# Kernel optimization log

Measured on AMD Instinct MI355X. Metric: run time of the kernel, lower is better.

## Reference

```python
import jax, jax.numpy as jnp
import numpy as np


def setup_inputs() -> dict:
    key = jax.random.key(0)
    ks = jax.random.split(key, 7)
    C = 256
    Cqk = C // 8  # 32
    B, D, H, W = 4, 16, 16, 16
    s_in = 1.0 / np.sqrt(C)  # conv1x1 fan_in = C
    return {
        "x": jax.random.normal(ks[0], (B, C, D, H, W), dtype=jnp.float32),
        "Wq": jax.random.uniform(ks[1], (Cqk, C), jnp.float32, -s_in, s_in),
        "bq": jax.random.uniform(ks[2], (Cqk,), jnp.float32, -s_in, s_in),
        "Wk": jax.random.uniform(ks[3], (Cqk, C), jnp.float32, -s_in, s_in),
        "bk": jax.random.uniform(ks[4], (Cqk,), jnp.float32, -s_in, s_in),
        "Wv": jax.random.uniform(ks[5], (C, C), jnp.float32, -s_in, s_in),
        "bv": jax.random.uniform(ks[6], (C,), jnp.float32, -s_in, s_in),
    }


def reference(x, Wq, bq, Wk, bk, Wv, bv):
    B, C, D, H, W = x.shape
    N = D * H * W
    xf = x.reshape(B, C, N)  # [B, C, N]
    # 1x1x1 convs == per-voxel GEMMs over the channel dim
    q = jnp.einsum('oc,bcn->bon', Wq, xf) + bq[None, :, None]  # [B, Cqk, N]
    k = jnp.einsum('oc,bcn->bon', Wk, xf) + bk[None, :, None]  # [B, Cqk, N]
    v = jnp.einsum('oc,bcn->bon', Wv, xf) + bv[None, :, None]  # [B, C, N]
    # attention[b, n, m] = softmax_m( q[:, n] . k[:, m] )
    scores = jnp.einsum('bcn,bcm->bnm', q, k)  # [B, N, N]
    attn = jax.nn.softmax(scores, axis=-1)
    # out = value @ attention^T  -> out[b, c, n] = sum_m v[b,c,m] * attn[b,n,m]
    out = jnp.einsum('bcm,bnm->bcn', v, attn)
    return x + out.reshape(B, C, D, H, W)
```

## Files before the change

### kernel.cpp

```cpp
#include <hip/hip_runtime.h>
#include <math.h>

#define B_   4
#define C_   256
#define CQK  32
#define N_   4096
#define TQ   64
#define TM   128
#define HIT2 (N_ / TM)
#define PSS  136
#define XTS  264

typedef __attribute__((ext_vector_type(8))) short short8;
typedef __attribute__((ext_vector_type(4))) short short4v;
typedef __attribute__((ext_vector_type(4))) float f32x4;
typedef __attribute__((ext_vector_type(2))) unsigned int uint2v;

#if __has_builtin(__builtin_amdgcn_exp2f)
#define EXP2F(x) __builtin_amdgcn_exp2f(x)
#else
#define EXP2F(x) exp2f(x)
#endif

__device__ __forceinline__ unsigned short f2bf(float f) {
    unsigned u = __builtin_bit_cast(unsigned, f);
    u += 0x7fffu + ((u >> 16) & 1u);
    return (unsigned short)(u >> 16);
}
__device__ __forceinline__ float bf2f(unsigned short s) {
    return __builtin_bit_cast(float, (unsigned)s << 16);
}
__device__ __forceinline__ unsigned pack2bf(float a, float b) {
    unsigned ua = __builtin_bit_cast(unsigned, a) + 0x8000u;
    unsigned ub = __builtin_bit_cast(unsigned, b) + 0x8000u;
#if __has_builtin(__builtin_amdgcn_perm)
    return __builtin_amdgcn_perm(ub, ua, 0x07060302u);
#else
    return (ua >> 16) | (ub & 0xffff0000u);
#endif
}

__global__ __launch_bounds__(256) void cvt_w(
    const float* __restrict__ Wq, const float* __restrict__ bq,
    const float* __restrict__ Wk, const float* __restrict__ bk,
    const float* __restrict__ Wv, const float* __restrict__ bv,
    unsigned short* __restrict__ wbf, float* __restrict__ biasf)
{
    const float LOG2E = 1.4426950408889634f;
    const int r = blockIdx.x;
    const int t = threadIdx.x;
    const float* src = (r < 32) ? (Wq + r * C_)
                     : (r < 64) ? (Wk + (r - 32) * C_)
                                : (Wv + (r - 64) * C_);
    const float scale = (r < 32) ? LOG2E : 1.0f;
    wbf[r * C_ + t] = f2bf(src[t] * scale);
    if (t == 0)
        biasf[r] = (r < 32) ? bq[r] * LOG2E : (r < 64) ? bk[r - 32] : bv[r - 64];
}

__global__ __launch_bounds__(256, 2) void proj_qkv(
    const float* __restrict__ x, const unsigned short* __restrict__ wbf,
    const float* __restrict__ biasf,
    unsigned short* __restrict__ qb, unsigned short* __restrict__ kb,
    unsigned short* __restrict__ vb)
{
    __shared__ __align__(16) unsigned short xT[64 * XTS];
    __shared__ __align__(16) unsigned short qks[64 * 72];

    const int t    = threadIdx.x;
    const int w    = t >> 6;
    const int lane = t & 63;
    const int quad = lane >> 4;
    const int c16  = lane & 15;
    const int n0   = blockIdx.x * 64;
    const int b    = blockIdx.y;

#pragma unroll
    for (int p = 0; p < 16; ++p) {
        const int c  = (t >> 2) + 64 * (p >> 2);
        const int nq = (t & 3) + 4 * (p & 3);
        const f32x4 xv = *(const f32x4*)&x[((size_t)(b * C_) + c) * N_ + n0 + 4 * nq];
#pragma unroll
        for (int j = 0; j < 4; ++j)
            xT[(4 * nq + j) * XTS + c] = f2bf(xv[j]);
    }
    __syncthreads();

    f32x4 acc[5][4];
#pragma unroll
    for (int i = 0; i < 5; ++i)
#pragma unroll
        for (int nt = 0; nt < 4; ++nt) acc[i][nt] = (f32x4){0.f, 0.f, 0.f, 0.f};

    const unsigned short* wr = wbf + (size_t)(80 * w + c16) * C_ + quad * 8;

#pragma unroll
    for (int ks = 0; ks < 8; ++ks) {
        short8 af[5], bf[4];
#pragma unroll
        for (int i = 0; i < 5; ++i)
            af[i] = *(const short8*)(wr + (size_t)(16 * i) * C_ + 32 * ks);
#pragma unroll
        for (int nt = 0; nt < 4; ++nt)
            bf[nt] = *(const short8*)&xT[(16 * nt + c16) * XTS + ks * 32 + quad * 8];
#pragma unroll
        for (int i = 0; i < 5; ++i)
#pragma unroll
            for (int nt = 0; nt < 4; ++nt)
                acc[i][nt] = __builtin_amdgcn_mfma_f32_16x16x32_bf16(af[i], bf[nt], acc[i][nt], 0, 0, 0);
    }

#pragma unroll
    for (int i = 0; i < 5; ++i) {
        const int OT = 5 * w + i;
        const int obase = OT * 16 + 4 * quad;
        const f32x4 bv4 = *(const f32x4*)&biasf[obase];
#pragma unroll
        for (int nt = 0; nt < 4; ++nt) {
            const int n = n0 + 16 * nt + c16;
            float vals[4];
#pragma unroll
            for (int r = 0; r < 4; ++r) vals[r] = acc[i][nt][r] + bv4[r];
            if (OT >= 4) {
#pragma unroll
                for (int r = 0; r < 4; ++r)
                    vb[((size_t)(b * C_) + obase + r - 64) * N_ + n] = f2bf(vals[r]);
            } else {
                const int row = 16 * nt + c16;
                const int col = (OT < 2 ? 0 : 32) + (OT & 1) * 16 + 4 * quad;
                short4v pk;
#pragma unroll
                for (int r = 0; r < 4; ++r) pk[r] = (short)f2bf(vals[r]);
                *(short4v*)&qks[row * 72 + col] = pk;
            }
        }
    }
    __syncthreads();
    if (w < 2) {
        unsigned short* dst = w ? kb : qb;
        const int coff = w ? 32 : 0;
#pragma unroll
        for (int h = 0; h < 4; ++h) {
            const int n = 16 * h + (lane >> 2);
            const int c = (lane & 3) * 8;
            const short8 v = *(const short8*)&qks[n * 72 + coff + c];
            *(short8*)(dst + ((size_t)(b * N_) + n0 + n) * 32 + c) = v;
        }
    }
}

__global__ __launch_bounds__(512, 2) void attn_kernel(
    const unsigned short* __restrict__ qg,
    const unsigned short* __restrict__ kg,
    const unsigned short* __restrict__ vg,
    const float* __restrict__ x,
    float* __restrict__ out)
{
    __shared__ __align__(16) unsigned short ks[TM * 40];
    __shared__ __align__(16) unsigned short vs[C_ * TM];
    __shared__ __align__(16) unsigned short ps[TQ * PSS];
    __shared__ float ls[8 * TQ];
    __shared__ float linv[TQ];

    const int t    = threadIdx.x;
    const int w    = t >> 6;
    const int lane = t & 63;
    const int quad = lane >> 4;
    const int c16  = lane & 15;
    const int flat = blockIdx.x;
    const int b    = flat & 3;
    const int q0   = (flat >> 2) * TQ;
    const int cs = w & 3;
    const int pg = w >> 2;

    const unsigned short* kbase = kg + (size_t)(b * N_) * 32;
    const unsigned short* vbase = vg + (size_t)(b * C_) * N_;

    short8 bq[4];
#pragma unroll
    for (int g = 0; g < 4; ++g)
        bq[g] = *(const short8*)(qg + ((size_t)(b * N_) + q0 + 16 * g + c16) * 32 + quad * 8);

    const int vcr = t >> 4, vj = t & 15;
    const int kn = t >> 2, kseg = t & 3;

    short8 vpre[8], kpre;
#pragma unroll
    for (int p = 0; p < 8; ++p)
        vpre[p] = *(const short8*)(vbase + (size_t)(vcr + 32 * p) * N_ + vj * 8);
    kpre = *(const short8*)(kbase + (size_t)kn * 32 + kseg * 8);

    f32x4 O[4][2];
#pragma unroll
    for (int ct = 0; ct < 4; ++ct)
#pragma unroll
        for (int qt = 0; qt < 2; ++qt) O[ct][qt] = (f32x4){0.f, 0.f, 0.f, 0.f};

    float lacc[4] = {0.f, 0.f, 0.f, 0.f};

#pragma unroll 1
    for (int it = 0; it < HIT2; ++it) {
#pragma unroll
        for (int p = 0; p < 8; ++p) {
            const int c = vcr + 32 * p;
            *(short8*)&vs[c * TM + 8 * (vj ^ (c & 15))] = vpre[p];
        }
        *(short8*)&ks[kn * 40 + kseg * 8] = kpre;
        __syncthreads();

        const short8 ak = *(const short8*)&ks[(16 * w + c16) * 40 + quad * 8];
        const f32x4 z = {0.f, 0.f, 0.f, 0.f};
        f32x4 sf[4];
#pragma unroll
        for (int g = 0; g < 4; ++g)
            sf[g] = __builtin_amdgcn_mfma_f32_16x16x32_bf16(ak, bq[g], z, 0, 0, 0);

#pragma unroll
        for (int g = 0; g < 4; ++g) {
            float p[4];
#pragma unroll
            for (int r = 0; r < 4; ++r) p[r] = EXP2F(sf[g][r]);
            lacc[g] += (p[0] + p[1]) + (p[2] + p[3]);
            uint2v u;
            u.x = pack2bf(p[0], p[1]);
            u.y = pack2bf(p[2], p[3]);
            *(uint2v*)&ps[(16 * g + c16) * PSS + w * 16 + 4 * quad] = u;
        }
        __syncthreads();

        if (it < HIT2 - 1) {
            const int kv0n = (it + 1) * TM;
#pragma unroll
            for (int p = 0; p < 8; ++p)
                vpre[p] = *(const short8*)(vbase + (size_t)(vcr + 32 * p) * N_ + kv0n + vj * 8);
            kpre = *(const short8*)(kbase + (size_t)(kv0n + kn) * 32 + kseg * 8);
        }

        short8 bp[2][4];
#pragma unroll
        for (int qt = 0; qt < 2; ++qt)
#pragma unroll
            for (int s = 0; s < 4; ++s)
                bp[qt][s] = *(const short8*)&ps[(32 * pg + 16 * qt + c16) * PSS + 32 * s + 8 * quad];
#pragma unroll
        for (int s = 0; s < 4; ++s)
#pragma unroll
            for (int ct = 0; ct < 4; ++ct) {
                const int c = 64 * cs + 16 * ct + c16;
                const short8 av = *(const short8*)&vs[c * TM + 8 * ((4 * s + quad) ^ (c & 15))];
#pragma unroll
                for (int qt = 0; qt < 2; ++qt)
                    O[ct][qt] = __builtin_amdgcn_mfma_f32_16x16x32_bf16(av, bp[qt][s], O[ct][qt], 0, 0, 0);
            }
        __syncthreads();
    }

#pragma unroll
    for (int g = 0; g < 4; ++g) {
        lacc[g] += __shfl_xor(lacc[g], 16);
        lacc[g] += __shfl_xor(lacc[g], 32);
    }
    if (quad == 0) {
#pragma unroll
        for (int g = 0; g < 4; ++g)
            ls[w * TQ + 16 * g + c16] = lacc[g];
    }
    __syncthreads();
    if (w == 0) {
        float s = 0.f;
#pragma unroll
        for (int j = 0; j < 8; ++j) s += ls[j * TQ + lane];
        linv[lane] = 1.0f / s;
    }
    __syncthreads();

    const float* xb = x + (size_t)(b * C_) * N_;
    float* ob = out + (size_t)(b * C_) * N_;
    float li[2];
#pragma unroll
    for (int qt = 0; qt < 2; ++qt) li[qt] = linv[32 * pg + 16 * qt + c16];
#pragma unroll
    for (int ct = 0; ct < 4; ++ct)
#pragma unroll
        for (int qt = 0; qt < 2; ++qt) {
            const int n = q0 + 32 * pg + 16 * qt + c16;
#pragma unroll
            for (int r = 0; r < 4; ++r) {
                const int c = 64 * cs + 16 * ct + 4 * quad + r;
                const size_t idx = (size_t)c * N_ + n;
                ob[idx] = xb[idx] + O[ct][qt][r] * li[qt];
            }
        }
}

extern "C" void kernel_launch(void* const* d_in, const int* in_sizes, int n_in,
                              void* d_out, int out_size, void* d_ws, size_t ws_size,
                              hipStream_t stream) {
    const float* x  = (const float*)d_in[0];
    const float* Wq = (const float*)d_in[1];
    const float* bq = (const float*)d_in[2];
    const float* Wk = (const float*)d_in[3];
    const float* bk = (const float*)d_in[4];
    const float* Wv = (const float*)d_in[5];
    const float* bv = (const float*)d_in[6];
    float* out = (float*)d_out;

    unsigned short* ws16 = (unsigned short*)d_ws;
    unsigned short* qb  = ws16;
    unsigned short* kb  = qb + (size_t)B_ * N_ * 32;
    unsigned short* vb  = kb + (size_t)B_ * N_ * 32;
    unsigned short* wbf = vb + (size_t)B_ * C_ * N_;
    float* biasf = (float*)(wbf + 320 * C_);

    cvt_w<<<dim3(320), 256, 0, stream>>>(Wq, bq, Wk, bk, Wv, bv, wbf, biasf);
    proj_qkv<<<dim3(N_ / 64, B_), 256, 0, stream>>>(x, wbf, biasf, qb, kb, vb);
    attn_kernel<<<dim3(256), 512, 0, stream>>>(qb, kb, vb, x, out);
}
```

Baseline: 154.6 us.

## Halve query and key tiles in attention kernel to double grid occupancy

Reduces the attention query tile to 32 and key tile to 64, doubles the grid to 512 blocks and raises launch bounds to four blocks per CU. Warp roles are remapped so four warps compute the scores and each warp accumulates one 16-query strip across its channel slice. This aims to fill more CUs and raise occupancy to hide latency. In exchange, V is reloaded from global memory twice as often per query, and barriers are more frequent relative to the MFMA work.

```diff
diff --git a/kernel.cpp b/kernel.cpp
--- a/kernel.cpp
+++ b/kernel.cpp
@@ -5,10 +5,10 @@
 #define C_   256
 #define CQK  32
 #define N_   4096
-#define TQ   64
-#define TM   128
-#define HIT2 (N_ / TM)
-#define PSS  136
+#define TQ   32
+#define TM   64
+#define HIT3 (N_ / TM)
+#define PSS  72
 #define XTS  264
 
 typedef __attribute__((ext_vector_type(8))) short short8;
@@ -149,7 +149,7 @@
     }
 }
 
-__global__ __launch_bounds__(512, 2) void attn_kernel(
+__global__ __launch_bounds__(512, 4) void attn_kernel(
     const unsigned short* __restrict__ qg,
     const unsigned short* __restrict__ kg,
     const unsigned short* __restrict__ vg,
@@ -159,7 +159,7 @@
     __shared__ __align__(16) unsigned short ks[TM * 40];
     __shared__ __align__(16) unsigned short vs[C_ * TM];
     __shared__ __align__(16) unsigned short ps[TQ * PSS];
-    __shared__ float ls[8 * TQ];
+    __shared__ float ls[4 * TQ];
     __shared__ float linv[TQ];
 
     const int t    = threadIdx.x;
@@ -170,127 +170,105 @@
     const int flat = blockIdx.x;
     const int b    = flat & 3;
     const int q0   = (flat >> 2) * TQ;
+    const int f   = w & 3;
+    const int qg_ = w >> 2;
     const int cs = w & 3;
     const int pg = w >> 2;
 
     const unsigned short* kbase = kg + (size_t)(b * N_) * 32;
     const unsigned short* vbase = vg + (size_t)(b * C_) * N_;
 
-    short8 bq[4];
-#pragma unroll
-    for (int g = 0; g < 4; ++g)
-        bq[g] = *(const short8*)(qg + ((size_t)(b * N_) + q0 + 16 * g + c16) * 32 + quad * 8);
-
-    const int vcr = t >> 4, vj = t & 15;
+    const short8 bq = *(const short8*)(qg + ((size_t)(b * N_) + q0 + 16 * qg_ + c16) * 32 + quad * 8);
+
+    const int vc0 = t >> 3, vj = t & 7;
     const int kn = t >> 2, kseg = t & 3;
 
-    short8 vpre[8], kpre;
-#pragma unroll
-    for (int p = 0; p < 8; ++p)
-        vpre[p] = *(const short8*)(vbase + (size_t)(vcr + 32 * p) * N_ + vj * 8);
-    kpre = *(const short8*)(kbase + (size_t)kn * 32 + kseg * 8);
-
-    f32x4 O[4][2];
-#pragma unroll
-    for (int ct = 0; ct < 4; ++ct)
-#pragma unroll
-        for (int qt = 0; qt < 2; ++qt) O[ct][qt] = (f32x4){0.f, 0.f, 0.f, 0.f};
-
-    float lacc[4] = {0.f, 0.f, 0.f, 0.f};
+    short8 vpre[4], kpre;
+#pragma unroll
+    for (int p = 0; p < 4; ++p)
+        vpre[p] = *(const short8*)(vbase + (size_t)(vc0 + 64 * p) * N_ + vj * 8);
+    if (t < 256)
+        kpre = *(const short8*)(kbase + (size_t)kn * 32 + kseg * 8);
+
+    f32x4 O[4];
+#pragma unroll
+    for (int ct = 0; ct < 4; ++ct) O[ct] = (f32x4){0.f, 0.f, 0.f, 0.f};
+
+    float lacc = 0.f;
 
 #pragma unroll 1
-    for (int it = 0; it < HIT2; ++it) {
-#pragma unroll
-        for (int p = 0; p < 8; ++p) {
-            const int c = vcr + 32 * p;
-            *(short8*)&vs[c * TM + 8 * (vj ^ (c & 15))] = vpre[p];
-        }
-        *(short8*)&ks[kn * 40 + kseg * 8] = kpre;
+    for (int it = 0; it < HIT3; ++it) {
+#pragma unroll
+        for (int p = 0; p < 4; ++p) {
+            const int c = vc0 + 64 * p;
+            *(short8*)&vs[c * TM + 8 * (vj ^ (c & 7))] = vpre[p];
+        }
+        if (t < 256)
+            *(short8*)&ks[kn * 40 + kseg * 8] = kpre;
         __syncthreads();
 
-        const short8 ak = *(const short8*)&ks[(16 * w + c16) * 40 + quad * 8];
+        const short8 ak = *(const short8*)&ks[(16 * f + c16) * 40 + quad * 8];
         const f32x4 z = {0.f, 0.f, 0.f, 0.f};
-        f32x4 sf[4];
-#pragma unroll
-        for (int g = 0; g < 4; ++g)
-            sf[g] = __builtin_amdgcn_mfma_f32_16x16x32_bf16(ak, bq[g], z, 0, 0, 0);
-
-#pragma unroll
-        for (int g = 0; g < 4; ++g) {
+        const f32x4 sf = __builtin_amdgcn_mfma_f32_16x16x32_bf16(ak, bq, z, 0, 0, 0);
+
+        {
             float p[4];
 #pragma unroll
-            for (int r = 0; r < 4; ++r) p[r] = EXP2F(sf[g][r]);
-            lacc[g] += (p[0] + p[1]) + (p[2] + p[3]);
+            for (int r = 0; r < 4; ++r) p[r] = EXP2F(sf[r]);
+            lacc += (p[0] + p[1]) + (p[2] + p[3]);
             uint2v u;
             u.x = pack2bf(p[0], p[1]);
             u.y = pack2bf(p[2], p[3]);
-            *(uint2v*)&ps[(16 * g + c16) * PSS + w * 16 + 4 * quad] = u;
+            *(uint2v*)&ps[(16 * qg_ + c16) * PSS + f * 16 + 4 * quad] = u;
         }
         __syncthreads();
 
-        if (it < HIT2 - 1) {
+        if (it < HIT3 - 1) {
             const int kv0n = (it + 1) * TM;
 #pragma unroll
-            for (int p = 0; p < 8; ++p)
-                vpre[p] = *(const short8*)(vbase + (size_t)(vcr + 32 * p) * N_ + kv0n + vj * 8);
-            kpre = *(const short8*)(kbase + (size_t)(kv0n + kn) * 32 + kseg * 8);
-        }
-
-        short8 bp[2][4];
-#pragma unroll
-        for (int qt = 0; qt < 2; ++qt)
-#pragma unroll
-            for (int s = 0; s < 4; ++s)
-                bp[qt][s] = *(const short8*)&ps[(32 * pg + 16 * qt + c16) * PSS + 32 * s + 8 * quad];
-#pragma unroll
-        for (int s = 0; s < 4; ++s)
+            for (int p = 0; p < 4; ++p)
+                vpre[p] = *(const short8*)(vbase + (size_t)(vc0 + 64 * p) * N_ + kv0n + vj * 8);
+            if (t < 256)
+                kpre = *(const short8*)(kbase + (size_t)(kv0n + kn) * 32 + kseg * 8);
+        }
+
+        short8 bp[2];
+#pragma unroll
+        for (int s = 0; s < 2; ++s)
+            bp[s] = *(const short8*)&ps[(16 * pg + c16) * PSS + 32 * s + 8 * quad];
+#pragma unroll
+        for (int s = 0; s < 2; ++s)
 #pragma unroll
             for (int ct = 0; ct < 4; ++ct) {
                 const int c = 64 * cs + 16 * ct + c16;
-                const short8 av = *(const short8*)&vs[c * TM + 8 * ((4 * s + quad) ^ (c & 15))];
-#pragma unroll
-                for (int qt = 0; qt < 2; ++qt)
-                    O[ct][qt] = __builtin_amdgcn_mfma_f32_16x16x32_bf16(av, bp[qt][s], O[ct][qt], 0, 0, 0);
+                const short8 av = *(const short8*)&vs[c * TM + 8 * ((4 * s + quad) ^ (c & 7))];
+                O[ct] = __builtin_amdgcn_mfma_f32_16x16x32_bf16(av, bp[s], O[ct], 0, 0, 0);
             }
         __syncthreads();
     }
 
-#pragma unroll
-    for (int g = 0; g < 4; ++g) {
-        lacc[g] += __shfl_xor(lacc[g], 16);
-        lacc[g] += __shfl_xor(lacc[g], 32);
-    }
-    if (quad == 0) {
-#pragma unroll
-        for (int g = 0; g < 4; ++g)
-            ls[w * TQ + 16 * g + c16] = lacc[g];
-    }
-    __syncthreads();
-    if (w == 0) {
-        float s = 0.f;
-#pragma unroll
-        for (int j = 0; j < 8; ++j) s += ls[j * TQ + lane];
-        linv[lane] = 1.0f / s;
-    }
+    lacc += __shfl_xor(lacc, 16);
+    lacc += __shfl_xor(lacc, 32);
+    if (quad == 0)
+        ls[f * TQ + 16 * qg_ + c16] = lacc;
+    __syncthreads();
+    if (w == 0 && lane < TQ)
+        linv[lane] = 1.0f / (ls[lane] + ls[TQ + lane] + ls[2 * TQ + lane] + ls[3 * TQ + lane]);
     __syncthreads();
 
     const float* xb = x + (size_t)(b * C_) * N_;
     float* ob = out + (size_t)(b * C_) * N_;
-    float li[2];
-#pragma unroll
-    for (int qt = 0; qt < 2; ++qt) li[qt] = linv[32 * pg + 16 * qt + c16];
-#pragma unroll
-    for (int ct = 0; ct < 4; ++ct)
-#pragma unroll
-        for (int qt = 0; qt < 2; ++qt) {
-            const int n = q0 + 32 * pg + 16 * qt + c16;
-#pragma unroll
-            for (int r = 0; r < 4; ++r) {
-                const int c = 64 * cs + 16 * ct + 4 * quad + r;
-                const size_t idx = (size_t)c * N_ + n;
-                ob[idx] = xb[idx] + O[ct][qt][r] * li[qt];
-            }
-        }
+    const float li = linv[16 * pg + c16];
+    const int n = q0 + 16 * pg + c16;
+#pragma unroll
+    for (int ct = 0; ct < 4; ++ct) {
+#pragma unroll
+        for (int r = 0; r < 4; ++r) {
+            const int c = 64 * cs + 16 * ct + 4 * quad + r;
+            const size_t idx = (size_t)c * N_ + n;
+            ob[idx] = xb[idx] + O[ct][r] * li;
+        }
+    }
 }
 
 extern "C" void kernel_launch(void* const* d_in, const int* in_sizes, int n_in,
@@ -314,5 +292,5 @@
 
     cvt_w<<<dim3(320), 256, 0, stream>>>(Wq, bq, Wk, bk, Wv, bv, wbf, biasf);
     proj_qkv<<<dim3(N_ / 64, B_), 256, 0, stream>>>(x, wbf, biasf, qb, kb, vb);
-    attn_kernel<<<dim3(256), 512, 0, stream>>>(qb, kb, vb, x, out);
-}
+    attn_kernel<<<dim3(512), 512, 0, stream>>>(qb, kb, vb, x, out);
+}
```

Measured after the change: 174.9 us. 1.13x slower.
